# Performance work log

Hardware: AMD Instinct MI355X
Metric: run time of the kernel (lower is better)

The kernel has to match this reference:

```python
import jax, jax.numpy as jnp
import numpy as np

C = 128      # in channels
CO = 64      # out channels
G = 32       # group-norm groups
RES_IN = 32  # input resolution
RES_OUT = 64 # subdivided resolution
N = 20000    # active input voxels
EPS = 1e-5


def setup_inputs() -> dict:
    key = jax.random.key(0)
    ks = jax.random.split(key, 12)
    # unique active voxel coords at RES_IN (batch index 0, single instance)
    rng = np.random.default_rng(0)
    flat = rng.choice(RES_IN ** 3, size=N, replace=False)
    xyz = np.stack([flat // (RES_IN * RES_IN), (flat // RES_IN) % RES_IN, flat % RES_IN], axis=1)
    x_coords = jnp.asarray(np.concatenate([np.zeros((N, 1), np.int32), xyz.astype(np.int32)], axis=1))
    x_feats = jax.random.normal(ks[0], (N, C), dtype=jnp.float32)
    gn1_g = 1.0 + 0.1 * jax.random.normal(ks[1], (C,), dtype=jnp.float32)
    gn1_b = 0.1 * jax.random.normal(ks[2], (C,), dtype=jnp.float32)
    W1 = 0.05 * jax.random.normal(ks[3], (3, 3, 3, C, CO), dtype=jnp.float32)
    b1 = 0.01 * jax.random.normal(ks[4], (CO,), dtype=jnp.float32)
    gn2_g = 1.0 + 0.1 * jax.random.normal(ks[5], (CO,), dtype=jnp.float32)
    gn2_b = 0.1 * jax.random.normal(ks[6], (CO,), dtype=jnp.float32)
    W2 = 0.05 * jax.random.normal(ks[7], (3, 3, 3, CO, CO), dtype=jnp.float32)  # zero_module in source; random here to exercise math
    b2 = 0.01 * jax.random.normal(ks[8], (CO,), dtype=jnp.float32)
    Ws = 0.05 * jax.random.normal(ks[9], (C, CO), dtype=jnp.float32)   # 1x1 skip conv
    bs = 0.01 * jax.random.normal(ks[10], (CO,), dtype=jnp.float32)
    return dict(x_feats=x_feats, x_coords=x_coords, gn1_g=gn1_g, gn1_b=gn1_b,
                W1=W1, b1=b1, gn2_g=gn2_g, gn2_b=gn2_b, W2=W2, b2=b2, Ws=Ws, bs=bs)


def group_norm(f, g, b):
    # single-instance sparse group norm: stats per group over all points
    n, c = f.shape
    x = f.reshape(n, G, c // G)
    mu = jnp.mean(x, axis=(0, 2), keepdims=True)
    var = jnp.mean((x - mu) ** 2, axis=(0, 2), keepdims=True)
    return ((x - mu) * jax.lax.rsqrt(var + EPS)).reshape(n, c) * g + b


def subdivide(coords, feats):
    n = coords.shape[0]
    offs = jnp.stack(jnp.meshgrid(jnp.arange(2), jnp.arange(2), jnp.arange(2), indexing='ij'), -1).reshape(8, 3)
    xyz = coords[:, None, 1:] * 2 + offs[None].astype(coords.dtype)          # [n,8,3]
    bidx = jnp.broadcast_to(coords[:, None, :1], (n, 8, 1))
    new_coords = jnp.concatenate([bidx, xyz], axis=-1).reshape(n * 8, 4)
    return new_coords, jnp.repeat(feats, 8, axis=0)


def subm_conv3(coords, feats, W, b):
    # submanifold 3x3x3 sparse conv: scatter to padded dense grid, gather 27 neighbors per active site
    cin = feats.shape[1]
    grid = jnp.zeros((RES_OUT + 2, RES_OUT + 2, RES_OUT + 2, cin), feats.dtype)
    grid = grid.at[coords[:, 1] + 1, coords[:, 2] + 1, coords[:, 3] + 1].set(feats)
    acc = jnp.zeros((feats.shape[0], W.shape[-1]), feats.dtype)
    for i in range(3):
        for j in range(3):
            for k in range(3):
                nb = grid[coords[:, 1] + i, coords[:, 2] + j, coords[:, 3] + k]  # [n, cin]
                acc = acc + nb @ W[i, j, k]
    return acc + b


def reference(x_feats, x_coords, gn1_g, gn1_b, W1, b1, gn2_g, gn2_b, W2, b2, Ws, bs):
    h = jax.nn.silu(group_norm(x_feats, gn1_g, gn1_b))
    hc, hf = subdivide(x_coords, h)
    _, xf = subdivide(x_coords, x_feats)
    hf = subm_conv3(hc, hf, W1, b1)
    hf = jax.nn.silu(group_norm(hf, gn2_g, gn2_b))
    hf = subm_conv3(hc, hf, W2, b2)
    out = hf + (xf @ Ws + bs)  # residual + 1x1 skip conv (out_channels != channels)
    return out
```

## Files before the change

### kernel.cpp

```cpp
#include <hip/hip_runtime.h>
#include <hip/hip_bf16.h>
#include <math.h>

#define N_PTS 20000
#define C_IN 128
#define C_OUT 64
#define M_PTS (N_PTS*8)
#define EPS 1e-5f

typedef __attribute__((ext_vector_type(8))) short short8;
typedef __attribute__((ext_vector_type(4))) float float4v;

__device__ __forceinline__ ushort f2bf(float f){
    unsigned int i = __float_as_uint(f);
    unsigned int r = i + 0x7fffu + ((i >> 16) & 1u);
    return (ushort)(r >> 16);
}
__device__ __forceinline__ float bf2f(ushort u){ return __uint_as_float(((unsigned int)u) << 16); }
__device__ __forceinline__ float silu(float z){ return z / (1.f + expf(-z)); }
__device__ __forceinline__ int cmp5(int v){
    v &= 0x1249; v = (v | (v >> 2)) & 0x10C3; v = (v | (v >> 4)) & 0x100F; v = (v | (v >> 8)) & 0x1F;
    return v;
}


__global__ void __launch_bounds__(256) prep_kernel(
    const float* __restrict__ W1, const float* __restrict__ W2,
    ushort* __restrict__ Wt1, ushort* __restrict__ Wt2,
    int* __restrict__ pg, ushort* __restrict__ h, ushort* __restrict__ h2,
    const float* __restrict__ x, float* __restrict__ stats)
{
    const int b = blockIdx.x, tid = threadIdx.x;
    if (b < 2048){
        int idx = b * 256 + tid;
        int j = idx & 7, l = (idx >> 3) & 63, nb = (idx >> 9) & 3, kb = (idx >> 11) & 3, t = idx >> 13;
        int ci = kb * 32 + (l >> 4) * 8 + j, co = nb * 16 + (l & 15);
        int o = t >> 3, jj = t & 7;
        int ox = (o >> 2) & 1, oy = (o >> 1) & 1, oz = o & 1;
        int jx = (jj >> 2) & 1, jy = (jj >> 1) & 1, jz = jj & 1;
        float s = 0.f;
#pragma unroll
        for (int dx = -1; dx <= 1; dx++){
            if (((ox + dx) >> 1) != ox + jx - 1) continue;
#pragma unroll
            for (int dy = -1; dy <= 1; dy++){
                if (((oy + dy) >> 1) != oy + jy - 1) continue;
#pragma unroll
                for (int dz = -1; dz <= 1; dz++){
                    if (((oz + dz) >> 1) != oz + jz - 1) continue;
                    s += W1[((dx+1)*9 + (dy+1)*3 + (dz+1)) * (C_IN*64) + ci * 64 + co];
                }
            }
        }
        Wt1[idx] = f2bf(s);
    } else if (b < 2480){
        int idx = (b - 2048) * 256 + tid;
        int j = idx & 7, l = (idx >> 3) & 63, nb = (idx >> 9) & 3, kb = (idx >> 11) & 1, t = idx >> 12;
        int ci = kb * 32 + (l >> 4) * 8 + j, co = nb * 16 + (l & 15);
        Wt2[idx] = f2bf(W2[(t * C_OUT + ci) * 64 + co]);
    } else if (b < 2608){
        int i = (b - 2480) * 256 + tid;
        pg[i] = -1;
        if (b == 2480){
            if (tid < C_IN) h[(size_t)N_PTS * C_IN + tid] = 0;
            if (tid < 256){
                h2[(size_t)M_PTS * C_OUT + tid] = 0;
                h2[(size_t)M_PTS * C_OUT + 256 + tid] = 0;
            }
        }
    } else {
        __shared__ float ls[64];
        if (tid < 64) ls[tid] = 0.f;
        __syncthreads();
        const int g = tid & 31;
        const int r0 = (b - 2608) * 8 + (tid >> 5);
        float sum = 0.f, sq = 0.f;
        for (int r = r0; r < N_PTS; r += 4096){
            float4 v = *(const float4*)(x + (size_t)r * C_IN + g * 4);
            sum += v.x + v.y + v.z + v.w;
            sq  += v.x*v.x + v.y*v.y + v.z*v.z + v.w*v.w;
        }
        atomicAdd(&ls[g], sum);
        atomicAdd(&ls[32 + g], sq);
        __syncthreads();
        if (tid < 64) atomicAdd(&stats[tid], ls[tid]);
    }
}

__global__ void __launch_bounds__(256) scatter_kernel(
    const int* __restrict__ cds, int* __restrict__ pg)
{
    int i = blockIdx.x * 256 + threadIdx.x;
    if (i < N_PTS){
        const int* cd = cds + i * 4;
        pg[(cd[1] * 32 + cd[2]) * 32 + cd[3]] = i;
    }
}

__global__ void __launch_bounds__(1024) sort_kernel(
    int* __restrict__ pg, unsigned int* __restrict__ ordp)
{
    __shared__ int psum[1024];
    const int t = threadIdx.x;
    int cnt = 0;
    for (int i = 0; i < 32; i++){
        int m = t * 32 + i;
        int x = cmp5(m >> 2), y = cmp5(m >> 1), z = cmp5(m);
        cnt += (pg[(x * 32 + y) * 32 + z] >= 0) ? 1 : 0;
    }
    psum[t] = cnt;
    __syncthreads();
    for (int off = 1; off < 1024; off <<= 1){
        int v = (t >= off) ? psum[t - off] : 0;
        __syncthreads();
        psum[t] += v;
        __syncthreads();
    }
    int run = psum[t] - cnt;
    for (int i = 0; i < 32; i++){
        int m = t * 32 + i;
        int x = cmp5(m >> 2), y = cmp5(m >> 1), z = cmp5(m);
        int ci = (x * 32 + y) * 32 + z;
        int pi = pg[ci];
        if (pi >= 0){
            ordp[run] = ((unsigned int)pi << 15) | (unsigned int)((x << 10) | (y << 5) | z);
            pg[ci] = run;
            run++;
        }
    }
}

__global__ void __launch_bounds__(256) mid_kernel(
    const int* __restrict__ cds, const int* __restrict__ pg,
    const float* __restrict__ x, const float* __restrict__ stats,
    const float* __restrict__ g1, const float* __restrict__ b1, ushort* __restrict__ h,
    const float* __restrict__ Wsk, const float* __restrict__ bsk, float* __restrict__ s)
{
    __shared__ float w[C_IN * C_OUT];
    const int b = blockIdx.x, tid = threadIdx.x;
    if (b < 2500){
        int i = (b * 256 + tid) * 4;
        int row = i >> 7, c0 = i & 127;
        const int* cd = cds + row * 4;
        int rk = pg[(cd[1] * 32 + cd[2]) * 32 + cd[3]];
        int g = c0 >> 2;
        float mu = stats[g] * (1.0f / (N_PTS * 4.0f));
        float var = stats[32 + g] * (1.0f / (N_PTS * 4.0f)) - mu * mu;
        float rs = rsqrtf(var + EPS);
        float4 v = *(const float4*)(x + i);
        ushort4 o;
        o.x = f2bf(silu((v.x - mu) * rs * g1[c0+0] + b1[c0+0]));
        o.y = f2bf(silu((v.y - mu) * rs * g1[c0+1] + b1[c0+1]));
        o.z = f2bf(silu((v.z - mu) * rs * g1[c0+2] + b1[c0+2]));
        o.w = f2bf(silu((v.w - mu) * rs * g1[c0+3] + b1[c0+3]));
        *(ushort4*)(h + (size_t)rk * C_IN + c0) = o;
    } else {
        for (int j = tid; j < C_IN * C_OUT; j += 256) w[j] = Wsk[j];
        __syncthreads();
        int co = tid & 63, pr = tid >> 6;
        int p = (b - 2500) * 4 + pr;
        const int* cd = cds + p * 4;
        int rk = pg[(cd[1] * 32 + cd[2]) * 32 + cd[3]];
        const float* xr = x + (size_t)p * C_IN;
        float a = bsk[co];
        for (int cb = 0; cb < C_IN; cb += 4){
            float4 v = *(const float4*)(xr + cb);
            a += v.x * w[(cb+0)*64+co] + v.y * w[(cb+1)*64+co]
               + v.z * w[(cb+2)*64+co] + v.w * w[(cb+3)*64+co];
        }
        s[(size_t)rk * C_OUT + co] = a;
    }
}

__global__ void __launch_bounds__(256, 4) conv1_corner(
    const ushort* __restrict__ feat, const int* __restrict__ pg,
    const unsigned int* __restrict__ ordp, const ushort* __restrict__ Wt,
    const float* __restrict__ bias, ushort* __restrict__ hf1_bf,
    float* __restrict__ statsAcc)
{
    const int tid = threadIdx.x;
    const int wid = tid >> 6, l = tid & 63;
    const int r16 = l & 15, qd = l >> 4;
    const int b = blockIdx.x;
    const int tg = (b >> 6) * 8 + (b & 7);
    const int o  = (b >> 3) & 7;
    if (tg >= 79) return;
    const int tile = tg * 4 + wid;
    if (tile >= 313) return;
    const int mb = tile * 64;

    int slot = mb + l;
    int cs = slot < N_PTS ? slot : N_PTS - 1;
    int cell = (int)(ordp[cs] & 0x7FFFu);
    int px = (cell >> 10) & 31, py = (cell >> 5) & 31, pz = cell & 31;
    int ex0 = px + ((o >> 2) & 1) - 1;
    int ey0 = py + ((o >> 1) & 1) - 1;
    int ez0 = pz + (o & 1) - 1;

    int rows8[8];
#pragma unroll
    for (int j = 0; j < 8; j++){
        int cx = ex0 + ((j >> 2) & 1), cy = ey0 + ((j >> 1) & 1), cz = ez0 + (j & 1);
        int row = N_PTS;
        if ((unsigned)cx < 32u && (unsigned)cy < 32u && (unsigned)cz < 32u){
            int pi = pg[cx * 1024 + cy * 32 + cz];
            if (pi >= 0) row = pi;
        }
        rows8[j] = row;
    }

    float4v acc[16];
#pragma unroll
    for (int c = 0; c < 16; c++) acc[c] = 0.f;

#pragma unroll
    for (int j = 0; j < 8; j++){
        int fr0 = __shfl(rows8[j],      r16, 64);
        int fr1 = __shfl(rows8[j], 16 + r16, 64);
        int fr2 = __shfl(rows8[j], 32 + r16, 64);
        int fr3 = __shfl(rows8[j], 48 + r16, 64);
        const ushort* a0 = feat + (size_t)fr0 * C_IN + qd * 8;
        const ushort* a1 = feat + (size_t)fr1 * C_IN + qd * 8;
        const ushort* a2 = feat + (size_t)fr2 * C_IN + qd * 8;
        const ushort* a3 = feat + (size_t)fr3 * C_IN + qd * 8;
        const ushort* wt = Wt + (size_t)(o * 8 + j) * 8192 + l * 8;
#pragma unroll
        for (int kb = 0; kb < 4; kb++){
            short8 b0 = *(const short8*)(wt + (kb*4+0)*512);
            short8 b1 = *(const short8*)(wt + (kb*4+1)*512);
            short8 b2 = *(const short8*)(wt + (kb*4+2)*512);
            short8 b3 = *(const short8*)(wt + (kb*4+3)*512);
            short8 av0 = *(const short8*)(a0 + kb*32);
            short8 av1 = *(const short8*)(a1 + kb*32);
            short8 av2 = *(const short8*)(a2 + kb*32);
            short8 av3 = *(const short8*)(a3 + kb*32);
            acc[0]  = __builtin_amdgcn_mfma_f32_16x16x32_bf16(av0, b0, acc[0],  0, 0, 0);
            acc[1]  = __builtin_amdgcn_mfma_f32_16x16x32_bf16(av0, b1, acc[1],  0, 0, 0);
            acc[2]  = __builtin_amdgcn_mfma_f32_16x16x32_bf16(av0, b2, acc[2],  0, 0, 0);
            acc[3]  = __builtin_amdgcn_mfma_f32_16x16x32_bf16(av0, b3, acc[3],  0, 0, 0);
            acc[4]  = __builtin_amdgcn_mfma_f32_16x16x32_bf16(av1, b0, acc[4],  0, 0, 0);
            acc[5]  = __builtin_amdgcn_mfma_f32_16x16x32_bf16(av1, b1, acc[5],  0, 0, 0);
            acc[6]  = __builtin_amdgcn_mfma_f32_16x16x32_bf16(av1, b2, acc[6],  0, 0, 0);
            acc[7]  = __builtin_amdgcn_mfma_f32_16x16x32_bf16(av1, b3, acc[7],  0, 0, 0);
            acc[8]  = __builtin_amdgcn_mfma_f32_16x16x32_bf16(av2, b0, acc[8],  0, 0, 0);
            acc[9]  = __builtin_amdgcn_mfma_f32_16x16x32_bf16(av2, b1, acc[9],  0, 0, 0);
            acc[10] = __builtin_amdgcn_mfma_f32_16x16x32_bf16(av2, b2, acc[10], 0, 0, 0);
            acc[11] = __builtin_amdgcn_mfma_f32_16x16x32_bf16(av2, b3, acc[11], 0, 0, 0);
            acc[12] = __builtin_amdgcn_mfma_f32_16x16x32_bf16(av3, b0, acc[12], 0, 0, 0);
            acc[13] = __builtin_amdgcn_mfma_f32_16x16x32_bf16(av3, b1, acc[13], 0, 0, 0);
            acc[14] = __builtin_amdgcn_mfma_f32_16x16x32_bf16(av3, b2, acc[14], 0, 0, 0);
            acc[15] = __builtin_amdgcn_mfma_f32_16x16x32_bf16(av3, b3, acc[15], 0, 0, 0);
        }
    }

    float bsv[4] = { bias[r16], bias[16 + r16], bias[32 + r16], bias[48 + r16] };
    float ps[4] = {0,0,0,0}, pq[4] = {0,0,0,0};
#pragma unroll
    for (int rb = 0; rb < 4; rb++)
#pragma unroll
        for (int nb = 0; nb < 4; nb++)
#pragma unroll
            for (int rg = 0; rg < 4; rg++){
                int sl = rb * 16 + qd * 4 + rg;
                int pr = mb + sl;
                float v = acc[rb * 4 + nb][rg] + bsv[nb];
                if (pr < N_PTS){
                    hf1_bf[(size_t)(pr * 8 + o) * 64 + nb * 16 + r16] = f2bf(v);
                    ps[nb] += v; pq[nb] += v * v;
                }
            }
#pragma unroll
    for (int nb = 0; nb < 4; nb++){
        float s1 = ps[nb], s2 = pq[nb];
        s1 += __shfl_xor(s1, 16, 64); s2 += __shfl_xor(s2, 16, 64);
        s1 += __shfl_xor(s1, 32, 64); s2 += __shfl_xor(s2, 32, 64);
        if (qd == 0){
            atomicAdd(&statsAcc[64 + nb * 16 + r16], s1);
            atomicAdd(&statsAcc[128 + nb * 16 + r16], s2);
        }
    }
}

__global__ void __launch_bounds__(256, 4) conv2_corner(
    const ushort* __restrict__ feat, const int* __restrict__ pg,
    const unsigned int* __restrict__ ordp,
    const ushort* __restrict__ Wt, const float* __restrict__ bias,
    const float* __restrict__ skip, float* __restrict__ out)
{
    const int tid = threadIdx.x;
    const int wid = tid >> 6, l = tid & 63;
    const int r16 = l & 15, qd = l >> 4;
    const int b = blockIdx.x;
    const int tile = b >> 1;
    const int o = (b & 1) * 4 + wid;
    const int ox = (o >> 2) & 1, oy = (o >> 1) & 1, oz = o & 1;
    const int mb = tile * 64;

    int slot = mb + l;
    int cs = slot < N_PTS ? slot : N_PTS - 1;
    unsigned int op = ordp[cs];
    int sp = (int)(op >> 15);
    int cell = (int)(op & 0x7FFFu);
    int px = (cell >> 10) & 31, py = (cell >> 5) & 31, pz = cell & 31;
    int ex0 = px + ox - 1, ey0 = py + oy - 1, ez0 = pz + oz - 1;

    int pb[8];
#pragma unroll
    for (int j = 0; j < 8; j++){
        int cx = ex0 + ((j >> 2) & 1), cy = ey0 + ((j >> 1) & 1), cz = ez0 + (j & 1);
        int base = M_PTS;
        if ((unsigned)cx < 32u && (unsigned)cy < 32u && (unsigned)cz < 32u){
            int pi = pg[cx * 1024 + cy * 32 + cz];
            if (pi >= 0) base = pi * 8;
        }
        pb[j] = base;
    }

    float4v acc[16];
#pragma unroll
    for (int c = 0; c < 16; c++) acc[c] = 0.f;

#pragma unroll
    for (int t = 0; t < 27; t++){
        const int dx = t / 9 - 1, dy = (t / 3) % 3 - 1, dz = t % 3 - 1;
        int sx = ox + dx, sy = oy + dy, sz = oz + dz;
        int jx = (sx >> 1) - ox + 1, jy = (sy >> 1) - oy + 1, jz = (sz >> 1) - oz + 1;
        int opi = (sx & 1) * 4 + (sy & 1) * 2 + (sz & 1);
        int m00 = jz ? pb[1] : pb[0];
        int m01 = jz ? pb[3] : pb[2];
        int m10 = jz ? pb[5] : pb[4];
        int m11 = jz ? pb[7] : pb[6];
        int n0 = jy ? m01 : m00;
        int n1 = jy ? m11 : m10;
        int row = (jx ? n1 : n0) + opi;
        int fr0 = __shfl(row,      r16, 64);
        int fr1 = __shfl(row, 16 + r16, 64);
        int fr2 = __shfl(row, 32 + r16, 64);
        int fr3 = __shfl(row, 48 + r16, 64);
        const ushort* a0 = feat + (size_t)fr0 * C_OUT + qd * 8;
        const ushort* a1 = feat + (size_t)fr1 * C_OUT + qd * 8;
        const ushort* a2 = feat + (size_t)fr2 * C_OUT + qd * 8;
        const ushort* a3 = feat + (size_t)fr3 * C_OUT + qd * 8;
        const ushort* wt = Wt + (size_t)t * 4096 + l * 8;
#pragma unroll
        for (int kb = 0; kb < 2; kb++){
            short8 b0 = *(const short8*)(wt + (kb*4+0)*512);
            short8 b1 = *(const short8*)(wt + (kb*4+1)*512);
            short8 b2 = *(const short8*)(wt + (kb*4+2)*512);
            short8 b3 = *(const short8*)(wt + (kb*4+3)*512);
            short8 av0 = *(const short8*)(a0 + kb*32);
            short8 av1 = *(const short8*)(a1 + kb*32);
            short8 av2 = *(const short8*)(a2 + kb*32);
            short8 av3 = *(const short8*)(a3 + kb*32);
            acc[0]  = __builtin_amdgcn_mfma_f32_16x16x32_bf16(av0, b0, acc[0],  0, 0, 0);
            acc[1]  = __builtin_amdgcn_mfma_f32_16x16x32_bf16(av0, b1, acc[1],  0, 0, 0);
            acc[2]  = __builtin_amdgcn_mfma_f32_16x16x32_bf16(av0, b2, acc[2],  0, 0, 0);
            acc[3]  = __builtin_amdgcn_mfma_f32_16x16x32_bf16(av0, b3, acc[3],  0, 0, 0);
            acc[4]  = __builtin_amdgcn_mfma_f32_16x16x32_bf16(av1, b0, acc[4],  0, 0, 0);
            acc[5]  = __builtin_amdgcn_mfma_f32_16x16x32_bf16(av1, b1, acc[5],  0, 0, 0);
            acc[6]  = __builtin_amdgcn_mfma_f32_16x16x32_bf16(av1, b2, acc[6],  0, 0, 0);
            acc[7]  = __builtin_amdgcn_mfma_f32_16x16x32_bf16(av1, b3, acc[7],  0, 0, 0);
            acc[8]  = __builtin_amdgcn_mfma_f32_16x16x32_bf16(av2, b0, acc[8],  0, 0, 0);
            acc[9]  = __builtin_amdgcn_mfma_f32_16x16x32_bf16(av2, b1, acc[9],  0, 0, 0);
            acc[10] = __builtin_amdgcn_mfma_f32_16x16x32_bf16(av2, b2, acc[10], 0, 0, 0);
            acc[11] = __builtin_amdgcn_mfma_f32_16x16x32_bf16(av2, b3, acc[11], 0, 0, 0);
            acc[12] = __builtin_amdgcn_mfma_f32_16x16x32_bf16(av3, b0, acc[12], 0, 0, 0);
            acc[13] = __builtin_amdgcn_mfma_f32_16x16x32_bf16(av3, b1, acc[13], 0, 0, 0);
            acc[14] = __builtin_amdgcn_mfma_f32_16x16x32_bf16(av3, b2, acc[14], 0, 0, 0);
            acc[15] = __builtin_amdgcn_mfma_f32_16x16x32_bf16(av3, b3, acc[15], 0, 0, 0);
        }
    }

    float bsv[4] = { bias[r16], bias[16 + r16], bias[32 + r16], bias[48 + r16] };
#pragma unroll
    for (int rb = 0; rb < 4; rb++)
#pragma unroll
        for (int rg = 0; rg < 4; rg++){
            int sl = rb * 16 + qd * 4 + rg;
            int slt = mb + sl;
            if (slt < N_PTS){
                int spr = __shfl(sp, sl, 64);
                const float* sk = skip + (size_t)slt * 64;
#pragma unroll
                for (int nb = 0; nb < 4; nb++){
                    int co = nb * 16 + r16;
                    out[(size_t)(spr * 8 + o) * 64 + co] = acc[rb * 4 + nb][rg] + bsv[nb] + sk[co];
                }
            }
        }
}

__global__ void __launch_bounds__(256) h2_kernel(
    const ushort* __restrict__ hf1, const float* __restrict__ stats,
    const float* __restrict__ gg, const float* __restrict__ gb, ushort* __restrict__ h2)
{
    int i = (blockIdx.x * 256 + threadIdx.x) * 4;
    if (i >= M_PTS * C_OUT) return;
    int c0 = i & (C_OUT - 1);
    const float inv = 1.0f / (M_PTS * 2.0f);
    float muA = (stats[64 + c0] + stats[64 + c0 + 1]) * inv;
    float vA  = (stats[128 + c0] + stats[128 + c0 + 1]) * inv - muA * muA;
    float rsA = rsqrtf(vA + EPS);
    float muB = (stats[64 + c0 + 2] + stats[64 + c0 + 3]) * inv;
    float vB  = (stats[128 + c0 + 2] + stats[128 + c0 + 3]) * inv - muB * muB;
    float rsB = rsqrtf(vB + EPS);
    ushort4 u = *(const ushort4*)(hf1 + i);
    ushort4 o;
    o.x = f2bf(silu((bf2f(u.x) - muA) * rsA * gg[c0+0] + gb[c0+0]));
    o.y = f2bf(silu((bf2f(u.y) - muA) * rsA * gg[c0+1] + gb[c0+1]));
    o.z = f2bf(silu((bf2f(u.z) - muB) * rsB * gg[c0+2] + gb[c0+2]));
    o.w = f2bf(silu((bf2f(u.w) - muB) * rsB * gg[c0+3] + gb[c0+3]));
    *(ushort4*)(h2 + i) = o;
}

extern "C" void kernel_launch(void* const* d_in, const int* in_sizes, int n_in,
                              void* d_out, int out_size, void* d_ws, size_t ws_size,
                              hipStream_t stream){
    const float* x   = (const float*)d_in[0];
    const int*   cds = (const int*)  d_in[1];
    const float* g1  = (const float*)d_in[2];
    const float* b1  = (const float*)d_in[3];
    const float* W1  = (const float*)d_in[4];
    const float* bb1 = (const float*)d_in[5];
    const float* g2  = (const float*)d_in[6];
    const float* b2  = (const float*)d_in[7];
    const float* W2  = (const float*)d_in[8];
    const float* bb2 = (const float*)d_in[9];
    const float* Wsk = (const float*)d_in[10];
    const float* bsk = (const float*)d_in[11];
    float* out = (float*)d_out;
    char* ws = (char*)d_ws;

    float*  stats = (float*) (ws);
    int*    pg    = (int*)   (ws + 1024);
    ushort* h     = (ushort*)(ws + 132096);
    ushort* h2    = (ushort*)(ws + 5252352);
    float*  s     = (float*) (ws + 25733376);
    ushort* Wt1   = (ushort*)(ws + 30853376);
    ushort* Wt2   = (ushort*)(ws + 31901952);
    unsigned int* ordp = (unsigned int*)(ws + 32123136);

    hipMemsetAsync(stats, 0, 192 * sizeof(float), stream);
    prep_kernel<<<3120, 256, 0, stream>>>(W1, W2, Wt1, Wt2, pg, h, h2, x, stats);
    scatter_kernel<<<79, 256, 0, stream>>>(cds, pg);
    sort_kernel<<<1, 1024, 0, stream>>>(pg, ordp);
    mid_kernel<<<7500, 256, 0, stream>>>(cds, pg, x, stats, g1, b1, h, Wsk, bsk, s);
    conv1_corner<<<640, 256, 0, stream>>>(h, pg, ordp, Wt1, bb1, (ushort*)d_out, stats);
    h2_kernel<<<12500, 256, 0, stream>>>((const ushort*)d_out, stats, g2, b2, h2);
    conv2_corner<<<626, 256, 0, stream>>>(h2, pg, ordp, Wt2, bb2, s, out);
}
```

Baseline: 402.0 us.

## Stage Morton-block halo of features in LDS for conv1 and split sort

Measured after the change: 399.4 us. No clear change (-0.7%).

```diff
diff --git a/kernel.cpp b/kernel.cpp
--- a/kernel.cpp
+++ b/kernel.cpp
@@ -97,26 +97,40 @@
     }
 }
 
-__global__ void __launch_bounds__(1024) sort_kernel(
-    int* __restrict__ pg, unsigned int* __restrict__ ordp)
-{
-    __shared__ int psum[1024];
-    const int t = threadIdx.x;
-    int cnt = 0;
+__global__ void __launch_bounds__(64) sortA_kernel(
+    const int* __restrict__ pg, int* __restrict__ cnt)
+{
+    int t = blockIdx.x * 64 + threadIdx.x;
+    int c = 0;
     for (int i = 0; i < 32; i++){
         int m = t * 32 + i;
         int x = cmp5(m >> 2), y = cmp5(m >> 1), z = cmp5(m);
-        cnt += (pg[(x * 32 + y) * 32 + z] >= 0) ? 1 : 0;
-    }
-    psum[t] = cnt;
+        c += (pg[(x * 32 + y) * 32 + z] >= 0) ? 1 : 0;
+    }
+    cnt[t] = c;
+}
+__global__ void __launch_bounds__(1024) sortB_kernel(
+    const int* __restrict__ cnt, int* __restrict__ base)
+{
+    __shared__ int ps[1024];
+    const int t = threadIdx.x;
+    int c = cnt[t];
+    ps[t] = c;
     __syncthreads();
     for (int off = 1; off < 1024; off <<= 1){
-        int v = (t >= off) ? psum[t - off] : 0;
+        int v = (t >= off) ? ps[t - off] : 0;
         __syncthreads();
-        psum[t] += v;
+        ps[t] += v;
         __syncthreads();
     }
-    int run = psum[t] - cnt;
+    base[t] = ps[t] - c;
+}
+__global__ void __launch_bounds__(64) sortC_kernel(
+    int* __restrict__ pg, unsigned int* __restrict__ ordp,
+    const int* __restrict__ base)
+{
+    int t = blockIdx.x * 64 + threadIdx.x;
+    int run = base[t];
     for (int i = 0; i < 32; i++){
         int m = t * 32 + i;
         int x = cmp5(m >> 2), y = cmp5(m >> 1), z = cmp5(m);
@@ -172,41 +186,67 @@
     }
 }
 
-__global__ void __launch_bounds__(256, 4) conv1_corner(
+#define HROWS 217
+#define HPITCH 136
+__global__ void __launch_bounds__(512, 4) conv1_halo(
     const ushort* __restrict__ feat, const int* __restrict__ pg,
-    const unsigned int* __restrict__ ordp, const ushort* __restrict__ Wt,
-    const float* __restrict__ bias, ushort* __restrict__ hf1_bf,
-    float* __restrict__ statsAcc)
-{
+    const unsigned int* __restrict__ ordp, const int* __restrict__ base,
+    const ushort* __restrict__ Wt, const float* __restrict__ bias,
+    ushort* __restrict__ hf1_bf, float* __restrict__ statsAcc)
+{
+    __shared__ ushort hstage[HROWS * HPITCH];
     const int tid = threadIdx.x;
-    const int wid = tid >> 6, l = tid & 63;
+    const int b = blockIdx.x;
+    const int t = (b & 7) * 64 + (b >> 3);
+    const int pbase = base[2 * t];
+    const int pend  = (t == 511) ? N_PTS : base[2 * t + 2];
+    if (pbase >= pend) return;
+    const int m0 = t << 6;
+    const int hx0 = cmp5(m0 >> 2) - 1, hy0 = cmp5(m0 >> 1) - 1, hz0 = cmp5(m0) - 1;
+
+    {
+        int r = tid >> 1, half = tid & 1;
+        if (r < HROWS){
+            uint4* dst = (uint4*)(hstage + r * HPITCH + half * 64);
+            int rk = -1;
+            if (r < 216){
+                int lx = r / 36, ly = (r / 6) % 6, lz = r % 6;
+                int cx = hx0 + lx, cy = hy0 + ly, cz = hz0 + lz;
+                if ((unsigned)cx < 32u && (unsigned)cy < 32u && (unsigned)cz < 32u)
+                    rk = pg[cx * 1024 + cy * 32 + cz];
+            }
+            if (rk >= 0){
+                const uint4* src = (const uint4*)(feat + (size_t)rk * C_IN + half * 64);
+#pragma unroll
+                for (int i = 0; i < 8; i++) dst[i] = src[i];
+            } else {
+                uint4 zz; zz.x = zz.y = zz.z = zz.w = 0u;
+#pragma unroll
+                for (int i = 0; i < 8; i++) dst[i] = zz;
+            }
+        }
+    }
+    __syncthreads();
+
+    const int o = tid >> 6, l = tid & 63;
     const int r16 = l & 15, qd = l >> 4;
-    const int b = blockIdx.x;
-    const int tg = (b >> 6) * 8 + (b & 7);
-    const int o  = (b >> 3) & 7;
-    if (tg >= 79) return;
-    const int tile = tg * 4 + wid;
-    if (tile >= 313) return;
-    const int mb = tile * 64;
-
-    int slot = mb + l;
-    int cs = slot < N_PTS ? slot : N_PTS - 1;
-    int cell = (int)(ordp[cs] & 0x7FFFu);
-    int px = (cell >> 10) & 31, py = (cell >> 5) & 31, pz = cell & 31;
-    int ex0 = px + ((o >> 2) & 1) - 1;
-    int ey0 = py + ((o >> 1) & 1) - 1;
-    int ez0 = pz + (o & 1) - 1;
+    const int ox = (o >> 2) & 1, oy = (o >> 1) & 1, oz = o & 1;
 
     int rows8[8];
-#pragma unroll
-    for (int j = 0; j < 8; j++){
-        int cx = ex0 + ((j >> 2) & 1), cy = ey0 + ((j >> 1) & 1), cz = ez0 + (j & 1);
-        int row = N_PTS;
-        if ((unsigned)cx < 32u && (unsigned)cy < 32u && (unsigned)cz < 32u){
-            int pi = pg[cx * 1024 + cy * 32 + cz];
-            if (pi >= 0) row = pi;
-        }
-        rows8[j] = row;
+    {
+        int valid = (pbase + l) < pend;
+        int cell = (int)(ordp[valid ? (pbase + l) : pbase] & 0x7FFFu);
+        int lx = ((cell >> 10) & 31) - hx0;
+        int ly = ((cell >> 5) & 31) - hy0;
+        int lz = (cell & 31) - hz0;
+#pragma unroll
+        for (int j = 0; j < 8; j++){
+            int nx = lx + ox - 1 + ((j >> 2) & 1);
+            int ny = ly + oy - 1 + ((j >> 1) & 1);
+            int nz = lz + oz - 1 + (j & 1);
+            int idx = (nx * 6 + ny) * 6 + nz;
+            rows8[j] = (valid ? idx : 216) * (HPITCH * 2);
+        }
     }
 
     float4v acc[16];
@@ -219,10 +259,10 @@
         int fr1 = __shfl(rows8[j], 16 + r16, 64);
         int fr2 = __shfl(rows8[j], 32 + r16, 64);
         int fr3 = __shfl(rows8[j], 48 + r16, 64);
-        const ushort* a0 = feat + (size_t)fr0 * C_IN + qd * 8;
-        const ushort* a1 = feat + (size_t)fr1 * C_IN + qd * 8;
-        const ushort* a2 = feat + (size_t)fr2 * C_IN + qd * 8;
-        const ushort* a3 = feat + (size_t)fr3 * C_IN + qd * 8;
+        const ushort* a0 = (const ushort*)((const char*)hstage + fr0) + qd * 8;
+        const ushort* a1 = (const ushort*)((const char*)hstage + fr1) + qd * 8;
+        const ushort* a2 = (const ushort*)((const char*)hstage + fr2) + qd * 8;
+        const ushort* a3 = (const ushort*)((const char*)hstage + fr3) + qd * 8;
         const ushort* wt = Wt + (size_t)(o * 8 + j) * 8192 + l * 8;
 #pragma unroll
         for (int kb = 0; kb < 4; kb++){
@@ -262,9 +302,9 @@
 #pragma unroll
             for (int rg = 0; rg < 4; rg++){
                 int sl = rb * 16 + qd * 4 + rg;
-                int pr = mb + sl;
+                int pr = pbase + sl;
                 float v = acc[rb * 4 + nb][rg] + bsv[nb];
-                if (pr < N_PTS){
+                if (pr < pend){
                     hf1_bf[(size_t)(pr * 8 + o) * 64 + nb * 16 + r16] = f2bf(v);
                     ps[nb] += v; pq[nb] += v * v;
                 }
@@ -308,12 +348,12 @@
 #pragma unroll
     for (int j = 0; j < 8; j++){
         int cx = ex0 + ((j >> 2) & 1), cy = ey0 + ((j >> 1) & 1), cz = ez0 + (j & 1);
-        int base = M_PTS;
+        int base_ = M_PTS;
         if ((unsigned)cx < 32u && (unsigned)cy < 32u && (unsigned)cz < 32u){
             int pi = pg[cx * 1024 + cy * 32 + cz];
-            if (pi >= 0) base = pi * 8;
-        }
-        pb[j] = base;
+            if (pi >= 0) base_ = pi * 8;
+        }
+        pb[j] = base_;
     }
 
     float4v acc[16];
@@ -439,13 +479,18 @@
     ushort* Wt1   = (ushort*)(ws + 30853376);
     ushort* Wt2   = (ushort*)(ws + 31901952);
     unsigned int* ordp = (unsigned int*)(ws + 32123136);
+    int*    cnt   = (int*)   (ws + 32203136);
+    int*    base  = (int*)   (ws + 32207232);
 
     hipMemsetAsync(stats, 0, 192 * sizeof(float), stream);
     prep_kernel<<<3120, 256, 0, stream>>>(W1, W2, Wt1, Wt2, pg, h, h2, x, stats);
     scatter_kernel<<<79, 256, 0, stream>>>(cds, pg);
-    sort_kernel<<<1, 1024, 0, stream>>>(pg, ordp);
+    sortA_kernel<<<16, 64, 0, stream>>>(pg, cnt);
+    sortB_kernel<<<1, 1024, 0, stream>>>(cnt, base);
+    sortC_kernel<<<16, 64, 0, stream>>>(pg, ordp, base);
     mid_kernel<<<7500, 256, 0, stream>>>(cds, pg, x, stats, g1, b1, h, Wsk, bsk, s);
-    conv1_corner<<<640, 256, 0, stream>>>(h, pg, ordp, Wt1, bb1, (ushort*)d_out, stats);
+    conv1_halo<<<512, 512, 0, stream>>>(h, pg, ordp, base, Wt1, bb1,
+                                        (ushort*)d_out, stats);
     h2_kernel<<<12500, 256, 0, stream>>>((const ushort*)d_out, stats, g2, b2, h2);
     conv2_corner<<<626, 256, 0, stream>>>(h2, pg, ordp, Wt2, bb2, s, out);
 }
```
